# Kernel tuning notes

Hardware: AMD Instinct MI355X
Metric: run time of the kernel (lower is better)

## Reference

```python
import jax, jax.numpy as jnp
import numpy as np

B, S, D, H = 8, 512, 1024, 8
DPH = D // H            # 128, dim per head
MAX_REL = 32
NGRAM = 2               # 2-gram RNN on heads 4..7
NG_START, NG_COUNT = 4, 4
SCALE = float(DPH) ** 0.5


def setup_inputs() -> dict:
    key = jax.random.key(0)
    ks = jax.random.split(key, 12)
    w = lambda k, shp: jax.random.normal(k, shp, jnp.float32) * 0.02
    return {
        "x": jax.random.normal(ks[0], (B, S, D), jnp.float32),
        "mask": jax.random.randint(ks[1], (B, 1, S), 0, 2).astype(bool),
        "Wq": w(ks[2], (D, D)), "bq": jnp.zeros((D,), jnp.float32),
        "Wk": w(ks[3], (D, D)), "bk": jnp.zeros((D,), jnp.float32),
        "Wv": w(ks[4], (D, D)), "bv": jnp.zeros((D,), jnp.float32),
        "Wo": w(ks[5], (D, D)), "bo": jnp.zeros((D,), jnp.float32),
        "rel_emb": w(ks[6], (2 * MAX_REL + 1, DPH)),
        "Wih_f": w(ks[7], (DPH, DPH)), "Whh_f": w(ks[8], (DPH, DPH)),
        "bih_f": jnp.zeros((DPH,), jnp.float32), "bhh_f": jnp.zeros((DPH,), jnp.float32),
        "Wih_b": w(ks[9], (DPH, DPH)), "Whh_b": w(ks[10], (DPH, DPH)),
        "bih_b": jnp.zeros((DPH,), jnp.float32), "bhh_b": jnp.zeros((DPH,), jnp.float32),
    }


def reference(x, mask, Wq, bq, Wk, bk, Wv, bv, Wo, bo, rel_emb,
              Wih_f, Whh_f, bih_f, bhh_f, Wih_b, Whh_b, bih_b, bhh_b):
    shape_h = lambda t: t.reshape(B, S, H, DPH).transpose(0, 2, 1, 3)  # [B,H,S,d]
    q = shape_h(x @ Wq.T + bq)
    k = shape_h(x @ Wk.T + bk)
    v = shape_h(x @ Wv.T + bv)

    # --- ngram path: zero masked positions in q/k/v (all heads) ---
    m = mask[:, :, :, None]  # [B,1,S,1] broadcast over heads and d
    q = jnp.where(m, 0.0, q)
    k = jnp.where(m, 0.0, k)
    v = jnp.where(m, 0.0, v)

    # per-head 2-gram bidirectional RNN on heads NG_START..NG_START+NG_COUNT-1
    qh = q[:, NG_START:NG_START + NG_COUNT].reshape(-1, S, DPH)
    kh = k[:, NG_START:NG_START + NG_COUNT].reshape(-1, S, DPH)
    vh = v[:, NG_START:NG_START + NG_COUNT].reshape(-1, S, DPH)
    feats = jnp.concatenate([qh, kh, vh], axis=0)          # [3*B*NG_COUNT, S, d]
    shifted = jnp.pad(feats, ((0, 0), (1, 0), (0, 0)))[:, :-1]  # shift-by-1 (prev token)
    seq = jnp.stack([shifted, feats], axis=0).reshape(NGRAM, -1, DPH)  # [T, N*S, d]
    h0 = jnp.zeros((seq.shape[1], DPH), jnp.float32)
    fstep = lambda h, xt: (jnp.tanh(xt @ Wih_f.T + bih_f + h @ Whh_f.T + bhh_f), None)
    bstep = lambda h, xt: (jnp.tanh(xt @ Wih_b.T + bih_b + h @ Whh_b.T + bhh_b), None)
    hf, _ = jax.lax.scan(fstep, h0, seq)            # fwd final hidden
    hb, _ = jax.lax.scan(bstep, h0, seq[::-1])      # bwd final hidden
    yy = (hf + hb).reshape(3, B, NG_COUNT, S, DPH)  # sum of direction finals
    q = q.at[:, NG_START:NG_START + NG_COUNT].set(yy[0])
    k = k.at[:, NG_START:NG_START + NG_COUNT].set(yy[1])
    v = v.at[:, NG_START:NG_START + NG_COUNT].set(yy[2])

    # --- relative-position attention ---
    qs = q / SCALE
    r = jnp.arange(S)
    rel_idx = jnp.clip(r[None, :] - r[:, None], -MAX_REL, MAX_REL) + MAX_REL  # [S,S]
    rel_k = rel_emb[rel_idx]  # [S,S,d]; same table used for keys and values
    scores = jnp.einsum('bhqd,bhkd->bhqk', qs, k) + jnp.einsum('bhqd,qkd->bhqk', qs, rel_k)
    scores = jnp.where(mask[:, None], -1e18, scores)  # [B,1,1,S] broadcast
    attn = jax.nn.softmax(scores, axis=-1)
    ctx = jnp.einsum('bhqk,bhkd->bhqd', attn, v) + jnp.einsum('bhqk,qkd->bhqd', attn, rel_k)
    out = ctx.transpose(0, 2, 1, 3).reshape(B, S, D) @ Wo.T + bo
    return out, attn
```

## Files before the change

kernel.cpp:

```cpp
#include <hip/hip_runtime.h>


typedef __bf16 bf16x8 __attribute__((ext_vector_type(8)));
typedef float f32x4 __attribute__((ext_vector_type(4)));

#define MFMA16(a, b, c) __builtin_amdgcn_mfma_f32_16x16x32_bf16(a, b, c, 0, 0, 0)

__device__ __forceinline__ unsigned short f2bf(float f) {
  unsigned u = __float_as_uint(f);
  u += 0x7FFFu + ((u >> 16) & 1u);
  return (unsigned short)(u >> 16);
}
__device__ __forceinline__ uint2 pack4(float4 f) {
  uint2 r;
  r.x = (unsigned)f2bf(f.x) | ((unsigned)f2bf(f.y) << 16);
  r.y = (unsigned)f2bf(f.z) | ((unsigned)f2bf(f.w) << 16);
  return r;
}
__device__ __forceinline__ void gld16(const unsigned short* g, unsigned short* l) {
  __builtin_amdgcn_global_load_lds(
      (const __attribute__((address_space(1))) unsigned int*)g,
      (__attribute__((address_space(3))) unsigned int*)l, 16, 0, 0);
}

__global__ __launch_bounds__(256) void prep_bf16(
    const float* __restrict__ x,
    const float* __restrict__ Wq, const float* __restrict__ Wk,
    const float* __restrict__ Wv,
    const float* __restrict__ Wihf, const float* __restrict__ Whhf,
    const float* __restrict__ Wihb, const float* __restrict__ Whhb,
    unsigned short* __restrict__ xb, unsigned short* __restrict__ Wqkvb,
    unsigned short* __restrict__ Wrnnb) {
  int i = blockIdx.x * 256 + threadIdx.x;
  const float* src;
  unsigned short* dst;
  int off;
  if (i < 1048576) {
    src = x; dst = xb; off = i;
  } else if (i < 1310720) {
    src = Wq; dst = Wqkvb; off = i - 1048576;
  } else if (i < 1572864) {
    src = Wk; dst = Wqkvb + 1048576; off = i - 1310720;
  } else if (i < 1835008) {
    src = Wv; dst = Wqkvb + 2097152; off = i - 1572864;
  } else if (i < 1839104) {
    src = Wihf; dst = Wrnnb; off = i - 1835008;
  } else if (i < 1843200) {
    src = Whhf; dst = Wrnnb + 16384; off = i - 1839104;
  } else if (i < 1847296) {
    src = Wihb; dst = Wrnnb + 32768; off = i - 1843200;
  } else {
    src = Whhb; dst = Wrnnb + 49152; off = i - 1847296;
  }
  float4 f = *((const float4*)src + off);
  *(uint2*)(dst + (size_t)off * 4) = pack4(f);
}

__global__ __launch_bounds__(256) void qkv_proj(
    const unsigned short* __restrict__ xb, const unsigned short* __restrict__ Wqkvb,
    const float* __restrict__ bq, const float* __restrict__ bk,
    const float* __restrict__ bv, const int* __restrict__ mask,
    unsigned short* __restrict__ qb, unsigned short* __restrict__ kb,
    unsigned short* __restrict__ vb, unsigned short* __restrict__ vT) {
  __shared__ __align__(16) unsigned short As[128 * 64];
  __shared__ __align__(16) unsigned short Bs[128 * 64];
  const int bm = blockIdx.x & 31;
  const int bn = blockIdx.x >> 5;
  const int t = bn >> 3;
  const int nloc0 = (bn & 7) * 128;
  const unsigned short* W = Wqkvb + (size_t)t * 1048576;
  const float* bias = (t == 0) ? bq : (t == 1) ? bk : bv;
  const int tid = threadIdx.x;
  const int lane = tid & 63, w = tid >> 6;
  const int wm = (w >> 1) * 64, wn = (w & 1) * 64;
  const int lanelo = lane & 15, quad = lane >> 4;
  const int row0 = bm * 128;
  const int rloc = lane >> 3, pch = lane & 7;
  const int lch = (pch - rloc) & 7;

  f32x4 acc[4][4];
  const f32x4 zf = {0.f, 0.f, 0.f, 0.f};
#pragma unroll
  for (int i = 0; i < 4; ++i)
#pragma unroll
    for (int j = 0; j < 4; ++j) acc[i][j] = zf;

  for (int kt = 0; kt < 16; ++kt) {
#pragma unroll
    for (int q = 0; q < 4; ++q) {
      int seg = w * 4 + q;
      int grow = seg * 8 + rloc;
      gld16(xb + (size_t)(row0 + grow) * 1024 + kt * 64 + lch * 8, &As[seg * 512]);
      gld16(W + (size_t)(nloc0 + grow) * 1024 + kt * 64 + lch * 8, &Bs[seg * 512]);
    }
    __syncthreads();
#pragma unroll
    for (int ks = 0; ks < 2; ++ks) {
      const int pA = (ks * 4 + quad + lanelo) & 7;
      bf16x8 a[4], bb[4];
#pragma unroll
      for (int i = 0; i < 4; ++i)
        a[i] = *(const bf16x8*)(&As[(wm + i * 16 + lanelo) * 64 + pA * 8]);
#pragma unroll
      for (int j = 0; j < 4; ++j)
        bb[j] = *(const bf16x8*)(&Bs[(wn + j * 16 + lanelo) * 64 + pA * 8]);
#pragma unroll
      for (int i = 0; i < 4; ++i)
#pragma unroll
        for (int j = 0; j < 4; ++j) acc[i][j] = MFMA16(a[i], bb[j], acc[i][j]);
    }
    __syncthreads();
  }
#pragma unroll
  for (int i = 0; i < 4; ++i) {
#pragma unroll
    for (int j = 0; j < 4; ++j) {
      int jj = nloc0 + wn + j * 16 + lanelo;
      int hh = jj >> 7, dc = jj & 127;
      float bvv = bias[jj];
      int m0 = row0 + wm + i * 16 + quad * 4;
      int b0 = m0 >> 9, sS = m0 & 511;
      unsigned short ov[4];
#pragma unroll
      for (int r = 0; r < 4; ++r) {
        int s = sS + r;
        float val = acc[i][j][r] + bvv;
        if (mask[b0 * 512 + s]) val = 0.f;
        unsigned short o = f2bf(val);
        ov[r] = o;
        size_t off = ((size_t)(b0 * 8 + hh) * 512 + s) * 128 + dc;
        if (t == 0) qb[off] = o;
        else if (t == 1) kb[off] = o;
        else vb[off] = o;
      }
      if (t == 2) {
        uint2 pk;
        pk.x = (unsigned)ov[0] | ((unsigned)ov[1] << 16);
        pk.y = (unsigned)ov[2] | ((unsigned)ov[3] << 16);
        *(uint2*)(&vT[((size_t)(b0 * 8 + hh) * 128 + dc) * 512 + sS]) = pk;
      }
    }
  }
}

__global__ __launch_bounds__(256) void prep_rel(
    const float* __restrict__ rel, unsigned short* __restrict__ relb,
    unsigned short* __restrict__ relT) {
  int i = blockIdx.x * 256 + threadIdx.x;
  if (i < 65 * 128) relb[i] = f2bf(rel[i]);
  if (i < 128 * 96) {
    int d = i / 96, r = i - d * 96;
    relT[i] = (r < 65) ? f2bf(rel[r * 128 + d]) : (unsigned short)0;
  }
}

__global__ __launch_bounds__(256) void rnn_fused(
    const unsigned short* __restrict__ qb, const unsigned short* __restrict__ kb,
    const unsigned short* __restrict__ vb,
    const unsigned short* __restrict__ Wrnnb,
    const float* __restrict__ bihf, const float* __restrict__ bhhf,
    const float* __restrict__ bihb, const float* __restrict__ bhhb,
    unsigned short* __restrict__ rnn_out) {
  __shared__ __align__(16) unsigned short X[65 * 136];
  __shared__ __align__(16) unsigned short H1[64 * 136];
  __shared__ float cbf[128], cbb[128];

  const unsigned short* Wihfb = Wrnnb;
  const unsigned short* Whhfb = Wrnnb + 16384;
  const unsigned short* Wihbb = Wrnnb + 32768;
  const unsigned short* Whhbb = Wrnnb + 49152;

  const int gid = blockIdx.x;
  const int tile = gid & 7;
  const int g = gid >> 3;
  const int t = g >> 5;
  const int rem = g & 31;
  const int b = rem >> 2, h = (rem & 3) + 4;
  const int s0 = tile * 64;
  const unsigned short* src = (t == 0) ? qb : (t == 1) ? kb : vb;
  const size_t rowbase = (size_t)(b * 8 + h) * 512;
  const int tid = threadIdx.x;

  for (int c = tid; c < 65 * 16; c += 256) {
    int r = c >> 4, cc = c & 15;
    uint4 v4;
    if (r == 0 && s0 == 0) v4 = make_uint4(0, 0, 0, 0);
    else v4 = *(const uint4*)(src + (rowbase + (s0 - 1 + r)) * 128 + cc * 8);
    *(uint4*)(&X[r * 136 + cc * 8]) = v4;
  }
  if (tid < 128) {
    cbf[tid] = bihf[tid] + bhhf[tid];
    cbb[tid] = bihb[tid] + bhhb[tid];
  }
  __syncthreads();

  const int lane = tid & 63, w = tid >> 6;
  const int lanelo = lane & 15, quad = lane >> 4;
  const int marow = w * 16 + lanelo;
  const int wfoff = lanelo * 128 + quad * 8;
  const f32x4 zf = {0.f, 0.f, 0.f, 0.f};


  f32x4 g1[8];
#pragma unroll
  for (int j = 0; j < 8; ++j) g1[j] = zf;
#pragma unroll
  for (int ks = 0; ks < 4; ++ks) {
    bf16x8 a = *(const bf16x8*)(&X[marow * 136 + ks * 32 + quad * 8]);
#pragma unroll
    for (int j = 0; j < 8; ++j) {
      bf16x8 bb = *(const bf16x8*)(Wihfb + j * 2048 + ks * 32 + wfoff);
      g1[j] = MFMA16(a, bb, g1[j]);
    }
  }
#pragma unroll
  for (int j = 0; j < 8; ++j) {
    int col = j * 16 + lanelo;
    float cb = cbf[col];
#pragma unroll
    for (int i = 0; i < 4; ++i) {
      int row = w * 16 + quad * 4 + i;
      H1[row * 136 + col] = f2bf(tanhf(g1[j][i] + cb));
    }
  }
  f32x4 a2[8];
#pragma unroll
  for (int j = 0; j < 8; ++j) a2[j] = zf;
#pragma unroll
  for (int ks = 0; ks < 4; ++ks) {
    bf16x8 a = *(const bf16x8*)(&X[(marow + 1) * 136 + ks * 32 + quad * 8]);
#pragma unroll
    for (int j = 0; j < 8; ++j) {
      bf16x8 bb = *(const bf16x8*)(Wihfb + j * 2048 + ks * 32 + wfoff);
      a2[j] = MFMA16(a, bb, a2[j]);
    }
  }
#pragma unroll
  for (int ks = 0; ks < 4; ++ks) {
    bf16x8 a = *(const bf16x8*)(&H1[marow * 136 + ks * 32 + quad * 8]);
#pragma unroll
    for (int j = 0; j < 8; ++j) {
      bf16x8 bb = *(const bf16x8*)(Whhfb + j * 2048 + ks * 32 + wfoff);
      a2[j] = MFMA16(a, bb, a2[j]);
    }
  }
  float outF[8][4];
#pragma unroll
  for (int j = 0; j < 8; ++j) {
    int col = j * 16 + lanelo;
    float cb = cbf[col];
#pragma unroll
    for (int i = 0; i < 4; ++i) outF[j][i] = tanhf(a2[j][i] + cb);
  }
#pragma unroll
  for (int j = 0; j < 8; ++j) g1[j] = zf;
#pragma unroll
  for (int ks = 0; ks < 4; ++ks) {
    bf16x8 a = *(const bf16x8*)(&X[(marow + 1) * 136 + ks * 32 + quad * 8]);
#pragma unroll
    for (int j = 0; j < 8; ++j) {
      bf16x8 bb = *(const bf16x8*)(Wihbb + j * 2048 + ks * 32 + wfoff);
      g1[j] = MFMA16(a, bb, g1[j]);
    }
  }
#pragma unroll
  for (int j = 0; j < 8; ++j) {
    int col = j * 16 + lanelo;
    float cb = cbb[col];
#pragma unroll
    for (int i = 0; i < 4; ++i) {
      int row = w * 16 + quad * 4 + i;
      H1[row * 136 + col] = f2bf(tanhf(g1[j][i] + cb));
    }
  }
#pragma unroll
  for (int j = 0; j < 8; ++j) a2[j] = zf;
#pragma unroll
  for (int ks = 0; ks < 4; ++ks) {
    bf16x8 a = *(const bf16x8*)(&X[marow * 136 + ks * 32 + quad * 8]);
#pragma unroll
    for (int j = 0; j < 8; ++j) {
      bf16x8 bb = *(const bf16x8*)(Wihbb + j * 2048 + ks * 32 + wfoff);
      a2[j] = MFMA16(a, bb, a2[j]);
    }
  }
#pragma unroll
  for (int ks = 0; ks < 4; ++ks) {
    bf16x8 a = *(const bf16x8*)(&H1[marow * 136 + ks * 32 + quad * 8]);
#pragma unroll
    for (int j = 0; j < 8; ++j) {
      bf16x8 bb = *(const bf16x8*)(Whhbb + j * 2048 + ks * 32 + wfoff);
      a2[j] = MFMA16(a, bb, a2[j]);
    }
  }
#pragma unroll
  for (int j = 0; j < 8; ++j) {
    int col = j * 16 + lanelo;
    float cb = cbb[col];
#pragma unroll
    for (int i = 0; i < 4; ++i) {
      int row = w * 16 + quad * 4 + i;
      float val = outF[j][i] + tanhf(a2[j][i] + cb);
      rnn_out[((size_t)g * 512 + s0 + row) * 128 + col] = f2bf(val);
    }
  }
}

__global__ __launch_bounds__(256) void rnn_copyback(
    const unsigned short* __restrict__ rnn_out,
    unsigned short* __restrict__ qb, unsigned short* __restrict__ kb,
    unsigned short* __restrict__ vT) {
  int idx = blockIdx.x * 256 + threadIdx.x;
  int g = idx >> 16;
  int r2 = idx & 65535;
  int s = r2 >> 7, col = r2 & 127;
  int t = g >> 5, rem = g & 31, b = rem >> 2, h = (rem & 3) + 4;
  unsigned short val = rnn_out[idx];
  size_t off = ((size_t)(b * 8 + h) * 512 + s) * 128 + col;
  if (t == 0) qb[off] = val;
  else if (t == 1) kb[off] = val;
  else vT[((size_t)(b * 8 + h) * 128 + col) * 512 + s] = val;
}

__global__ __launch_bounds__(256) void scores_av_fused(
    const unsigned short* __restrict__ qbuf, const unsigned short* __restrict__ kbuf,
    const unsigned short* __restrict__ relb, const unsigned short* __restrict__ vT,
    const unsigned short* __restrict__ relT, const float* __restrict__ relf,
    const int* __restrict__ mask, float* __restrict__ attn_out,
    unsigned short* __restrict__ ctx) {
  __shared__ __align__(16) char smem[22528];
  unsigned short* As = (unsigned short*)smem;
  float* Ps = (float*)(smem + 4352);
  float* cmaskS = (float*)(smem + 9728);
  unsigned short* attnb = (unsigned short*)smem;
  unsigned short* abufT = (unsigned short*)(smem + 16384);
  float* redb = (float*)(smem + 18432);

  const int idx = blockIdx.x;
  const int qt = idx >> 6, bh = idx & 63, b = bh >> 3;
  const int q0 = qt * 16;
  const size_t qrow0 = (size_t)bh * 512 + q0;
  const int tid = threadIdx.x;
  const int lane = tid & 63, w = tid >> 6;
  const int lanelo = lane & 15, quad = lane >> 4;
  const f32x4 zf = {0.f, 0.f, 0.f, 0.f};

  {
    int r = tid >> 4, cc = tid & 15;
    *(uint4*)(&As[r * 136 + cc * 8]) = *(const uint4*)(qbuf + (qrow0 + r) * 128 + cc * 8);
  }
  for (int i = tid; i < 512; i += 256) cmaskS[i] = mask[b * 512 + i] ? -1e9f : 0.f;
  if (tid < 128) *(uint4*)(&abufT[tid * 8]) = make_uint4(0, 0, 0, 0);
  __syncthreads();

  if (w == 0) {
    f32x4 pacc[5];
#pragma unroll
    for (int j = 0; j < 5; ++j) pacc[j] = zf;
#pragma unroll
    for (int ks = 0; ks < 4; ++ks) {
      bf16x8 qf_ = *(const bf16x8*)(&As[lanelo * 136 + ks * 32 + quad * 8]);
#pragma unroll
      for (int j = 0; j < 5; ++j) {
        int r = j * 16 + lanelo;
        uint4 tmp = make_uint4(0, 0, 0, 0);
        if (r < 65) tmp = *(const uint4*)(relb + r * 128 + ks * 32 + quad * 8);
        bf16x8 rf_ = *(bf16x8*)&tmp;
        pacc[j] = MFMA16(rf_, qf_, pacc[j]);
      }
    }
#pragma unroll
    for (int j = 0; j < 5; ++j)
      *(f32x4*)(&Ps[lanelo * 84 + j * 16 + quad * 4]) = pacc[j];
  }
  __syncthreads();

  f32x4 acc[8];
#pragma unroll
  for (int kf = 0; kf < 8; ++kf) acc[kf] = zf;
  const unsigned short* kbp = kbuf + (size_t)bh * 65536;
#pragma unroll
  for (int ks = 0; ks < 4; ++ks) {
    bf16x8 qfr = *(const bf16x8*)(&As[lanelo * 136 + ks * 32 + quad * 8]);
    bf16x8 kfr[8];
#pragma unroll
    for (int kf = 0; kf < 8; ++kf)
      kfr[kf] = *(const bf16x8*)(kbp + (size_t)((w * 8 + kf) * 16 + lanelo) * 128 +
                                 ks * 32 + quad * 8);
#pragma unroll
    for (int kf = 0; kf < 8; ++kf) acc[kf] = MFMA16(kfr[kf], qfr, acc[kf]);
  }

  const float rscale = 0.08838834764831845f;
  float pmax = -3e38f;
  {
    const int q = lanelo;
    const int qg = q0 + q;
    const float* PsR = &Ps[q * 84];
    const float p0 = PsR[0], p64 = PsR[64];
#pragma unroll
    for (int kf = 0; kf < 8; ++kf) {
      const int kmin = w * 128 + kf * 16;
      const int kbase = kmin + quad * 4;
      if (kmin + 15 - q0 <= -32) {
#pragma unroll
        for (int i = 0; i < 4; ++i) {
          float val = (acc[kf][i] + p0) * rscale + cmaskS[kbase + i];
          acc[kf][i] = val;
          pmax = fmaxf(pmax, val);
        }
      } else if (kmin - (q0 + 15) >= 32) {
#pragma unroll
        for (int i = 0; i < 4; ++i) {
          float val = (acc[kf][i] + p64) * rscale + cmaskS[kbase + i];
          acc[kf][i] = val;
          pmax = fmaxf(pmax, val);
        }
      } else {
#pragma unroll
        for (int i = 0; i < 4; ++i) {
          int k = kbase + i;
          int d = k - qg;
          int r = min(max(d, -32), 32) + 32;
          float val = (acc[kf][i] + PsR[r]) * rscale + cmaskS[k];
          acc[kf][i] = val;
          pmax = fmaxf(pmax, val);
        }
      }
    }
  }
  float* red_max = redb;
  float* red_sum = redb + 256;
  float* red_s0 = redb + 512;
  float* red_s64 = redb + 768;
  pmax = fmaxf(pmax, __shfl_xor(pmax, 16, 64));
  pmax = fmaxf(pmax, __shfl_xor(pmax, 32, 64));
  if (quad == 0) red_max[w * 64 + lanelo] = pmax;
  __syncthreads();
  float mf_, psum = 0.f;
  {
    int q = lanelo;
    mf_ = fmaxf(fmaxf(red_max[q], red_max[64 + q]),
                fmaxf(red_max[128 + q], red_max[192 + q]));
  }
#pragma unroll
  for (int kf = 0; kf < 8; ++kf)
#pragma unroll
    for (int i = 0; i < 4; ++i) {
      float e = __expf(acc[kf][i] - mf_);
      acc[kf][i] = e;
      psum += e;
    }
  psum += __shfl_xor(psum, 16, 64);
  psum += __shfl_xor(psum, 32, 64);
  if (quad == 0) red_sum[w * 64 + lanelo] = psum;
  __syncthreads();
  float rs;
  {
    int q = lanelo;
    float s = red_sum[q] + red_sum[64 + q] + red_sum[128 + q] + red_sum[192 + q];
    rs = (s > 0.f) ? 1.f / s : 0.f;
  }

  float s0p = 0.f, s64p = 0.f;
  {
    const int q = lanelo;
    const int qg = q0 + q;
#pragma unroll
    for (int kf = 0; kf < 8; ++kf) {
      const int kmin = w * 128 + kf * 16;
      const int kbase = kmin + quad * 4;
      float4 at;
      float* ap = (float*)&at;
#pragma unroll
      for (int i = 0; i < 4; ++i) ap[i] = acc[kf][i] * rs;
      if (kmin + 15 - q0 <= -32) {
#pragma unroll
        for (int i = 0; i < 4; ++i) s0p += ap[i];
      } else if (kmin - (q0 + 15) >= 32) {
#pragma unroll
        for (int i = 0; i < 4; ++i) s64p += ap[i];
      } else {
#pragma unroll
        for (int i = 0; i < 4; ++i) {
          int d = kbase + i - qg;
          if (d <= -32) s0p += ap[i];
          else if (d >= 32) s64p += ap[i];
          else {
            int col = d + 32;
            abufT[q * 64 + (((col >> 3) + q) & 7) * 8 + (col & 7)] = f2bf(ap[i]);
          }
        }
      }
      *(float4*)(&attn_out[((size_t)bh * 512 + qg) * 512 + kbase]) = at;
      uint2 pk = pack4(at);
      int cc = kbase >> 3;
      *(uint2*)(&attnb[q * 512 + ((cc + q) & 63) * 8 + (quad & 1) * 4]) = pk;
    }
  }
  s0p += __shfl_xor(s0p, 16, 64);
  s0p += __shfl_xor(s0p, 32, 64);
  s64p += __shfl_xor(s64p, 16, 64);
  s64p += __shfl_xor(s64p, 32, 64);
  if (quad == 0) {
    red_s0[w * 64 + lanelo] = s0p;
    red_s64[w * 64 + lanelo] = s64p;
  }
  __syncthreads();
  float s0f, s64f;
  {
    int q = lanelo;
    s0f = red_s0[q] + red_s0[64 + q] + red_s0[128 + q] + red_s0[192 + q];
    s64f = red_s64[q] + red_s64[64 + q] + red_s64[128 + q] + red_s64[192 + q];
  }

  f32x4 cacc[2];
#pragma unroll
  for (int mf = 0; mf < 2; ++mf) cacc[mf] = zf;
  const unsigned short* vbp = vT + (size_t)bh * 65536;
#pragma unroll
  for (int kt = 0; kt < 16; ++kt) {
    bf16x8 afr[2], bfr;
#pragma unroll
    for (int mf = 0; mf < 2; ++mf)
      afr[mf] = *(const bf16x8*)(vbp + (size_t)((w * 2 + mf) * 16 + lanelo) * 512 +
                                 kt * 32 + quad * 8);
    {
      int q = lanelo;
      bfr = *(const bf16x8*)(&attnb[q * 512 + ((kt * 4 + quad + q) & 63) * 8]);
    }
#pragma unroll
    for (int mf = 0; mf < 2; ++mf) cacc[mf] = MFMA16(afr[mf], bfr, cacc[mf]);
  }
#pragma unroll
  for (int kt = 16; kt < 18; ++kt) {
    bf16x8 afr[2], bfr;
#pragma unroll
    for (int mf = 0; mf < 2; ++mf)
      afr[mf] = *(const bf16x8*)(relT + ((w * 2 + mf) * 16 + lanelo) * 96 +
                                 (kt - 16) * 32 + quad * 8);
    {
      int q = lanelo;
      bfr = *(const bf16x8*)(&abufT[q * 64 + (((kt - 16) * 4 + quad + q) & 7) * 8]);
    }
#pragma unroll
    for (int mf = 0; mf < 2; ++mf) cacc[mf] = MFMA16(afr[mf], bfr, cacc[mf]);
  }

  float r0v[2][4], r64v[2][4];
#pragma unroll
  for (int mf = 0; mf < 2; ++mf)
#pragma unroll
    for (int i = 0; i < 4; ++i) {
      int d = w * 32 + mf * 16 + quad * 4 + i;
      r0v[mf][i] = relf[d];
      r64v[mf][i] = relf[64 * 128 + d];
    }
  const int b_ = bh >> 3, h_ = bh & 7;
  {
    int qg = q0 + lanelo;
#pragma unroll
    for (int mf = 0; mf < 2; ++mf) {
      unsigned short ov[4];
#pragma unroll
      for (int i = 0; i < 4; ++i) {
        float val = cacc[mf][i] + s0f * r0v[mf][i] + s64f * r64v[mf][i];
        ov[i] = f2bf(val);
      }
      uint2 pk;
      pk.x = (unsigned)ov[0] | ((unsigned)ov[1] << 16);
      pk.y = (unsigned)ov[2] | ((unsigned)ov[3] << 16);
      *(uint2*)(&ctx[((size_t)(b_ * 512 + qg)) * 1024 + h_ * 128 + w * 32 + mf * 16 + quad * 4]) = pk;
    }
  }
}

__global__ __launch_bounds__(256) void out_proj(
    const unsigned short* __restrict__ ctx, const float* __restrict__ Wo,
    const float* __restrict__ bo, float* __restrict__ outp) {
  __shared__ __align__(16) unsigned short As[128 * 64];
  __shared__ __align__(16) unsigned short Bs[128 * 64];
  const int bm = blockIdx.x & 31, bn = blockIdx.x >> 5;
  const int tid = threadIdx.x, lane = tid & 63, w = tid >> 6;
  const int wm = (w >> 1) * 64, wn = (w & 1) * 64;
  const int lanelo = lane & 15, quad = lane >> 4;
  const int row0 = bm * 128, col0 = bn * 128;
  const int rloc = lane >> 3, pch = lane & 7;
  const int lch = (pch - rloc) & 7;
  f32x4 acc[4][4];
  const f32x4 zf = {0.f, 0.f, 0.f, 0.f};
#pragma unroll
  for (int i = 0; i < 4; ++i)
#pragma unroll
    for (int j = 0; j < 4; ++j) acc[i][j] = zf;

  for (int kt = 0; kt < 16; ++kt) {
#pragma unroll
    for (int q = 0; q < 4; ++q) {
      int seg = w * 4 + q;
      int grow = seg * 8 + rloc;
      gld16(ctx + (size_t)(row0 + grow) * 1024 + kt * 64 + lch * 8, &As[seg * 512]);
    }
    for (int c = tid; c < 1024; c += 256) {
      int r = c >> 3, cc2 = c & 7;
      const float* src = Wo + (size_t)(col0 + r) * 1024 + kt * 64 + cc2 * 8;
      int pc = (cc2 + r) & 7;
      *(uint2*)(&Bs[r * 64 + pc * 8]) = pack4(*(const float4*)src);
      *(uint2*)(&Bs[r * 64 + pc * 8 + 4]) = pack4(*(const float4*)(src + 4));
    }
    __syncthreads();
#pragma unroll
    for (int ks = 0; ks < 2; ++ks) {
      const int pA = (ks * 4 + quad + lanelo) & 7;
      bf16x8 a[4], bb[4];
#pragma unroll
      for (int i = 0; i < 4; ++i)
        a[i] = *(const bf16x8*)(&As[(wm + i * 16 + lanelo) * 64 + pA * 8]);
#pragma unroll
      for (int j = 0; j < 4; ++j)
        bb[j] = *(const bf16x8*)(&Bs[(wn + j * 16 + lanelo) * 64 + pA * 8]);
#pragma unroll
      for (int i = 0; i < 4; ++i)
#pragma unroll
        for (int j = 0; j < 4; ++j) acc[i][j] = MFMA16(a[i], bb[j], acc[i][j]);
    }
    __syncthreads();
  }
#pragma unroll
  for (int i = 0; i < 4; ++i) {
#pragma unroll
    for (int j = 0; j < 4; ++j) {
      int n = col0 + wn + j * 16 + lanelo;
      float bbv = bo[n];
#pragma unroll
      for (int r = 0; r < 4; ++r) {
        int m = row0 + wm + i * 16 + quad * 4 + r;
        outp[(size_t)m * 1024 + n] = acc[i][j][r] + bbv;
      }
    }
  }
}

extern "C" void kernel_launch(void* const* d_in, const int* in_sizes, int n_in,
                              void* d_out, int out_size, void* d_ws, size_t ws_size,
                              hipStream_t stream) {
  const float* x    = (const float*)d_in[0];
  const int*   mask = (const int*)d_in[1];
  const float* Wq   = (const float*)d_in[2];
  const float* bq   = (const float*)d_in[3];
  const float* Wk   = (const float*)d_in[4];
  const float* bk   = (const float*)d_in[5];
  const float* Wv   = (const float*)d_in[6];
  const float* bv   = (const float*)d_in[7];
  const float* Wo   = (const float*)d_in[8];
  const float* bo   = (const float*)d_in[9];
  const float* rel  = (const float*)d_in[10];
  const float* Wihf = (const float*)d_in[11];
  const float* Whhf = (const float*)d_in[12];
  const float* bihf = (const float*)d_in[13];
  const float* bhhf = (const float*)d_in[14];
  const float* Wihb = (const float*)d_in[15];
  const float* Whhb = (const float*)d_in[16];
  const float* bihb = (const float*)d_in[17];
  const float* bhhb = (const float*)d_in[18];

  char* ws = (char*)d_ws;
  unsigned short* qb   = (unsigned short*)(ws + 0);
  unsigned short* kb   = (unsigned short*)(ws + 8388608);
  unsigned short* vT   = (unsigned short*)(ws + 16777216);
  unsigned short* ctx  = (unsigned short*)(ws + 25165824);
  unsigned short* relb = (unsigned short*)(ws + 33554432);
  unsigned short* relT = (unsigned short*)(ws + 33571072);

  float* outp  = (float*)d_out;
  float* attnF = outp + 4194304;
  unsigned short* abase  = (unsigned short*)attnF;
  unsigned short* xb     = abase;
  unsigned short* vb     = abase + 4194304;
  unsigned short* rnnout = abase + 8388608;
  unsigned short* Wqkvb  = abase + 14680064;
  unsigned short* Wrnnb  = abase + 17825792;

  prep_bf16<<<dim3(7232), dim3(256), 0, stream>>>(
      x, Wq, Wk, Wv, Wihf, Whhf, Wihb, Whhb, xb, Wqkvb, Wrnnb);
  prep_rel<<<dim3(48), dim3(256), 0, stream>>>(rel, relb, relT);
  qkv_proj<<<dim3(768), dim3(256), 0, stream>>>(xb, Wqkvb, bq, bk, bv, mask,
                                                qb, kb, vb, vT);
  rnn_fused<<<dim3(768), dim3(256), 0, stream>>>(qb, kb, vb, Wrnnb,
                                                 bihf, bhhf, bihb, bhhb, rnnout);
  rnn_copyback<<<dim3(24576), dim3(256), 0, stream>>>(rnnout, qb, kb, vT);
  scores_av_fused<<<dim3(2048), dim3(256), 0, stream>>>(qb, kb, relb, vT, relT,
                                                        rel, mask, attnF, ctx);
  out_proj<<<dim3(256), dim3(256), 0, stream>>>(ctx, Wo, bo, outp);
}
```

Baseline: 412.6 us.

## Fuse RNN copyback into rnn_fused via saved tile-boundary rows

The qkv projection now saves each 64-token tile's last row for the n-gram heads into a small boundary buffer that aliases ctx. This lets rnn_fused write its results directly into q/k and the transposed vT in place without racing neighbouring tiles, which removes the separate rnn_copyback kernel and its intermediate buffer round trip. The MFMA loops that share a weight fragment are also merged so each B-fragment load feeds two accumulators. In exchange the kernel holds more live registers, and correctness depends on ctx not being used before scores_av_fused.

```diff
diff --git a/kernel.cpp b/kernel.cpp
--- a/kernel.cpp
+++ b/kernel.cpp
@@ -61,7 +61,8 @@
     const float* __restrict__ bq, const float* __restrict__ bk,
     const float* __restrict__ bv, const int* __restrict__ mask,
     unsigned short* __restrict__ qb, unsigned short* __restrict__ kb,
-    unsigned short* __restrict__ vb, unsigned short* __restrict__ vT) {
+    unsigned short* __restrict__ vb, unsigned short* __restrict__ vT,
+    unsigned short* __restrict__ bnd) {
   __shared__ __align__(16) unsigned short As[128 * 64];
   __shared__ __align__(16) unsigned short Bs[128 * 64];
   const int bm = blockIdx.x & 31;
@@ -132,6 +133,8 @@
         if (t == 0) qb[off] = o;
         else if (t == 1) kb[off] = o;
         else vb[off] = o;
+        if (((s & 63) == 63) && s != 511 && hh >= 4)
+          bnd[((size_t)(t * 32 + b0 * 4 + (hh - 4)) * 7 + (s >> 6)) * 128 + dc] = o;
       }
       if (t == 2) {
         uint2 pk;
@@ -155,12 +158,12 @@
 }
 
 __global__ __launch_bounds__(256) void rnn_fused(
-    const unsigned short* __restrict__ qb, const unsigned short* __restrict__ kb,
+    unsigned short* __restrict__ qb, unsigned short* __restrict__ kb,
     const unsigned short* __restrict__ vb,
     const unsigned short* __restrict__ Wrnnb,
     const float* __restrict__ bihf, const float* __restrict__ bhhf,
     const float* __restrict__ bihb, const float* __restrict__ bhhb,
-    unsigned short* __restrict__ rnn_out) {
+    const unsigned short* __restrict__ bnd, unsigned short* __restrict__ vT) {
   __shared__ __align__(16) unsigned short X[65 * 136];
   __shared__ __align__(16) unsigned short H1[64 * 136];
   __shared__ float cbf[128], cbb[128];
@@ -184,8 +187,12 @@
   for (int c = tid; c < 65 * 16; c += 256) {
     int r = c >> 4, cc = c & 15;
     uint4 v4;
-    if (r == 0 && s0 == 0) v4 = make_uint4(0, 0, 0, 0);
-    else v4 = *(const uint4*)(src + (rowbase + (s0 - 1 + r)) * 128 + cc * 8);
+    if (r == 0) {
+      if (s0 == 0) v4 = make_uint4(0, 0, 0, 0);
+      else v4 = *(const uint4*)(bnd + ((size_t)g * 7 + (tile - 1)) * 128 + cc * 8);
+    } else {
+      v4 = *(const uint4*)(src + (rowbase + (s0 - 1 + r)) * 128 + cc * 8);
+    }
     *(uint4*)(&X[r * 136 + cc * 8]) = v4;
   }
   if (tid < 128) {
@@ -200,17 +207,19 @@
   const int wfoff = lanelo * 128 + quad * 8;
   const f32x4 zf = {0.f, 0.f, 0.f, 0.f};
 
-
-  f32x4 g1[8];
-#pragma unroll
-  for (int j = 0; j < 8; ++j) g1[j] = zf;
+  f32x4 g1[8], a2[8];
+#pragma unroll
+  for (int j = 0; j < 8; ++j) { g1[j] = zf; a2[j] = zf; }
+
 #pragma unroll
   for (int ks = 0; ks < 4; ++ks) {
-    bf16x8 a = *(const bf16x8*)(&X[marow * 136 + ks * 32 + quad * 8]);
+    bf16x8 ap = *(const bf16x8*)(&X[marow * 136 + ks * 32 + quad * 8]);
+    bf16x8 ac = *(const bf16x8*)(&X[(marow + 1) * 136 + ks * 32 + quad * 8]);
 #pragma unroll
     for (int j = 0; j < 8; ++j) {
       bf16x8 bb = *(const bf16x8*)(Wihfb + j * 2048 + ks * 32 + wfoff);
-      g1[j] = MFMA16(a, bb, g1[j]);
+      g1[j] = MFMA16(ap, bb, g1[j]);
+      a2[j] = MFMA16(ac, bb, a2[j]);
     }
   }
 #pragma unroll
@@ -223,18 +232,6 @@
       H1[row * 136 + col] = f2bf(tanhf(g1[j][i] + cb));
     }
   }
-  f32x4 a2[8];
-#pragma unroll
-  for (int j = 0; j < 8; ++j) a2[j] = zf;
-#pragma unroll
-  for (int ks = 0; ks < 4; ++ks) {
-    bf16x8 a = *(const bf16x8*)(&X[(marow + 1) * 136 + ks * 32 + quad * 8]);
-#pragma unroll
-    for (int j = 0; j < 8; ++j) {
-      bf16x8 bb = *(const bf16x8*)(Wihfb + j * 2048 + ks * 32 + wfoff);
-      a2[j] = MFMA16(a, bb, a2[j]);
-    }
-  }
 #pragma unroll
   for (int ks = 0; ks < 4; ++ks) {
     bf16x8 a = *(const bf16x8*)(&H1[marow * 136 + ks * 32 + quad * 8]);
@@ -253,14 +250,16 @@
     for (int i = 0; i < 4; ++i) outF[j][i] = tanhf(a2[j][i] + cb);
   }
 #pragma unroll
-  for (int j = 0; j < 8; ++j) g1[j] = zf;
+  for (int j = 0; j < 8; ++j) { g1[j] = zf; a2[j] = zf; }
 #pragma unroll
   for (int ks = 0; ks < 4; ++ks) {
-    bf16x8 a = *(const bf16x8*)(&X[(marow + 1) * 136 + ks * 32 + quad * 8]);
+    bf16x8 ap = *(const bf16x8*)(&X[marow * 136 + ks * 32 + quad * 8]);
+    bf16x8 ac = *(const bf16x8*)(&X[(marow + 1) * 136 + ks * 32 + quad * 8]);
 #pragma unroll
     for (int j = 0; j < 8; ++j) {
       bf16x8 bb = *(const bf16x8*)(Wihbb + j * 2048 + ks * 32 + wfoff);
-      g1[j] = MFMA16(a, bb, g1[j]);
+      g1[j] = MFMA16(ac, bb, g1[j]);
+      a2[j] = MFMA16(ap, bb, a2[j]);
     }
   }
 #pragma unroll
@@ -274,17 +273,6 @@
     }
   }
 #pragma unroll
-  for (int j = 0; j < 8; ++j) a2[j] = zf;
-#pragma unroll
-  for (int ks = 0; ks < 4; ++ks) {
-    bf16x8 a = *(const bf16x8*)(&X[marow * 136 + ks * 32 + quad * 8]);
-#pragma unroll
-    for (int j = 0; j < 8; ++j) {
-      bf16x8 bb = *(const bf16x8*)(Wihbb + j * 2048 + ks * 32 + wfoff);
-      a2[j] = MFMA16(a, bb, a2[j]);
-    }
-  }
-#pragma unroll
   for (int ks = 0; ks < 4; ++ks) {
     bf16x8 a = *(const bf16x8*)(&H1[marow * 136 + ks * 32 + quad * 8]);
 #pragma unroll
@@ -297,29 +285,25 @@
   for (int j = 0; j < 8; ++j) {
     int col = j * 16 + lanelo;
     float cb = cbb[col];
+    unsigned short ov[4];
 #pragma unroll
     for (int i = 0; i < 4; ++i) {
-      int row = w * 16 + quad * 4 + i;
       float val = outF[j][i] + tanhf(a2[j][i] + cb);
-      rnn_out[((size_t)g * 512 + s0 + row) * 128 + col] = f2bf(val);
-    }
-  }
-}
-
-__global__ __launch_bounds__(256) void rnn_copyback(
-    const unsigned short* __restrict__ rnn_out,
-    unsigned short* __restrict__ qb, unsigned short* __restrict__ kb,
-    unsigned short* __restrict__ vT) {
-  int idx = blockIdx.x * 256 + threadIdx.x;
-  int g = idx >> 16;
-  int r2 = idx & 65535;
-  int s = r2 >> 7, col = r2 & 127;
-  int t = g >> 5, rem = g & 31, b = rem >> 2, h = (rem & 3) + 4;
-  unsigned short val = rnn_out[idx];
-  size_t off = ((size_t)(b * 8 + h) * 512 + s) * 128 + col;
-  if (t == 0) qb[off] = val;
-  else if (t == 1) kb[off] = val;
-  else vT[((size_t)(b * 8 + h) * 128 + col) * 512 + s] = val;
+      ov[i] = f2bf(val);
+    }
+    int row0l = w * 16 + quad * 4;
+    if (t == 2) {
+      uint2 pk;
+      pk.x = (unsigned)ov[0] | ((unsigned)ov[1] << 16);
+      pk.y = (unsigned)ov[2] | ((unsigned)ov[3] << 16);
+      *(uint2*)(&vT[((size_t)(b * 8 + h) * 128 + col) * 512 + s0 + row0l]) = pk;
+    } else {
+      unsigned short* dst = (t == 0) ? qb : kb;
+#pragma unroll
+      for (int i = 0; i < 4; ++i)
+        dst[(rowbase + s0 + row0l + i) * 128 + col] = ov[i];
+    }
+  }
 }
 
 __global__ __launch_bounds__(256) void scores_av_fused(
@@ -671,13 +655,13 @@
   unsigned short* ctx  = (unsigned short*)(ws + 25165824);
   unsigned short* relb = (unsigned short*)(ws + 33554432);
   unsigned short* relT = (unsigned short*)(ws + 33571072);
+  unsigned short* bnd  = ctx;
 
   float* outp  = (float*)d_out;
   float* attnF = outp + 4194304;
   unsigned short* abase  = (unsigned short*)attnF;
   unsigned short* xb     = abase;
   unsigned short* vb     = abase + 4194304;
-  unsigned short* rnnout = abase + 8388608;
   unsigned short* Wqkvb  = abase + 14680064;
   unsigned short* Wrnnb  = abase + 17825792;
 
@@ -685,10 +669,9 @@
       x, Wq, Wk, Wv, Wihf, Whhf, Wihb, Whhb, xb, Wqkvb, Wrnnb);
   prep_rel<<<dim3(48), dim3(256), 0, stream>>>(rel, relb, relT);
   qkv_proj<<<dim3(768), dim3(256), 0, stream>>>(xb, Wqkvb, bq, bk, bv, mask,
-                                                qb, kb, vb, vT);
+                                                qb, kb, vb, vT, bnd);
   rnn_fused<<<dim3(768), dim3(256), 0, stream>>>(qb, kb, vb, Wrnnb,
-                                                 bihf, bhhf, bihb, bhhb, rnnout);
-  rnn_copyback<<<dim3(24576), dim3(256), 0, stream>>>(rnnout, qb, kb, vT);
+                                                 bihf, bhhf, bihb, bhhb, bnd, vT);
   scores_av_fused<<<dim3(2048), dim3(256), 0, stream>>>(qb, kb, relb, vT, relT,
                                                         rel, mask, attnF, ctx);
   out_proj<<<dim3(256), dim3(256), 0, stream>>>(ctx, Wo, bo, outp);
```

Measured after the change: 379.6 us. 1.09x faster.
